# Performance work log

Measured on AMD Instinct MI355X. Metric: run time of the kernel, lower is better.

## Reference

```python
import jax, jax.numpy as jnp
import numpy as np

B, T, D, NH = 2, 2048, 1024, 32
HD = D // NH  # 32
EPS = 1e-6


def rms_norm(x):
    # normalize over head dim in fp32, cast back
    ms = jnp.mean(x.astype(jnp.float32) ** 2, axis=-1, keepdims=True)
    return x * jax.lax.rsqrt(ms + EPS).astype(x.dtype)


def apply_rope(x, cos, sin):
    d = x.shape[-1] // 2
    x1, x2 = x[..., :d], x[..., d:]
    c = cos[: x.shape[-2], :d]
    s = sin[: x.shape[-2], :d]
    return jnp.concatenate([x1 * c - x2 * s, x2 * c + x1 * s], axis=-1)


def setup_inputs() -> dict:
    key = jax.random.key(0)
    ks = jax.random.split(key, 5)
    sc = 1.0 / np.sqrt(D)
    x = jax.random.normal(ks[0], (B, T, D), jnp.float32)
    Wq = jax.random.normal(ks[1], (D, D), jnp.float32) * sc
    Wk = jax.random.normal(ks[2], (NH * HD, D), jnp.float32) * sc
    Wv = jax.random.normal(ks[3], (NH * HD, D), jnp.float32) * sc
    Wproj = jax.random.normal(ks[4], (D, D), jnp.float32) * sc
    q_gain = jnp.ones((NH,), jnp.float32)  # qk_gain = 1.0
    # real RoPE tables, shape [T, HD//2]
    pos = np.arange(T, dtype=np.float32)
    inv = 1.0 / (10000.0 ** (np.arange(HD // 2, dtype=np.float32) / (HD // 2)))
    ang = pos[:, None] * inv[None, :]
    cos = jnp.asarray(np.cos(ang), jnp.float32)
    sin = jnp.asarray(np.sin(ang), jnp.float32)
    return {"x": x, "Wq": Wq, "Wk": Wk, "Wv": Wv, "Wproj": Wproj,
            "q_gain": q_gain, "cos": cos, "sin": sin}


def reference(x, Wq, Wk, Wv, Wproj, q_gain, cos, sin):
    Bx, Tx, Dx = x.shape
    nh = q_gain.shape[0]
    hd = Dx // nh
    # projections -> [B, H, T, hd]
    q = (x @ Wq.T).reshape(Bx, Tx, nh, hd).transpose(0, 2, 1, 3)
    k = (x @ Wk.T).reshape(Bx, Tx, nh, hd).transpose(0, 2, 1, 3)
    v = (x @ Wv.T).reshape(Bx, Tx, nh, hd).transpose(0, 2, 1, 3)
    q = apply_rope(rms_norm(q), cos, sin) * q_gain[None, :, None, None]
    k = apply_rope(rms_norm(k), cos, sin)
    scale = hd ** (-0.5)
    scores = jnp.einsum('bhqd,bhkd->bhqk', q, k) * scale
    causal = jnp.tril(jnp.ones((Tx, Tx), bool))
    scores = jnp.where(causal, scores, jnp.finfo(scores.dtype).min)
    attn = jax.nn.softmax(scores, axis=-1)
    y = jnp.einsum('bhqk,bhkd->bhqd', attn, v)
    y = y.transpose(0, 2, 1, 3).reshape(Bx, Tx, Dx)
    return y @ Wproj.T
```

## Files before the change

kernel.cpp:

```cpp
#include <hip/hip_runtime.h>

#define DEV __device__ __forceinline__

typedef __bf16 bf16x8 __attribute__((ext_vector_type(8)));
typedef float f32x4 __attribute__((ext_vector_type(4)));

static constexpr int Tn = 2048;
static constexpr int Dn = 1024;
static constexpr int NHn = 32;
static constexpr int Mn = 2 * Tn;
static constexpr float QSCALE = 0.17677669529663687f * 1.4426950408889634f;

DEV unsigned short f2bf(float f) {
    unsigned int u = __builtin_bit_cast(unsigned int, f);
    u = u + 0x7FFFu + ((u >> 16) & 1u);
    return (unsigned short)(u >> 16);
}

#define GPTR(p) ((const __attribute__((address_space(1))) void*)(p))
#define LPTR(p) ((__attribute__((address_space(3))) void*)(p))

__global__ __launch_bounds__(256) void cast_all(
    const float* __restrict__ x, const float* __restrict__ Wq, const float* __restrict__ Wk,
    const float* __restrict__ Wv, const float* __restrict__ Wp,
    unsigned short* __restrict__ xb, unsigned short* __restrict__ wall) {
    int i = blockIdx.x * 256 + threadIdx.x;
    const float* src;
    ushort4* dst;
    if (i < (1 << 20)) {
        src = x + (size_t)i * 4;
        dst = reinterpret_cast<ushort4*>(xb) + i;
    } else {
        int j = i - (1 << 20);
        int sel = j >> 18, off = j & ((1 << 18) - 1);
        const float* w = (sel == 0) ? Wq : (sel == 1) ? Wk : (sel == 2) ? Wv : Wp;
        src = w + (size_t)off * 4;
        dst = reinterpret_cast<ushort4*>(wall) + ((size_t)sel << 18) + off;
    }
    float4 v = *reinterpret_cast<const float4*>(src);
    ushort4 o;
    o.x = f2bf(v.x); o.y = f2bf(v.y); o.z = f2bf(v.z); o.w = f2bf(v.w);
    *dst = o;
}

__global__ __launch_bounds__(256) void gemm_qkv(
    const unsigned short* __restrict__ A, const unsigned short* __restrict__ Wall,
    unsigned short* __restrict__ Qn, unsigned short* __restrict__ Kn, unsigned short* __restrict__ Vt,
    const float* __restrict__ gain, const float* __restrict__ cosp, const float* __restrict__ sinp) {
    const int z = blockIdx.z;
    const unsigned short* Bm = Wall + (size_t)z * (Dn * Dn);
    const int m0 = blockIdx.x * 128, n0 = blockIdx.y * 128;
    const int tid = threadIdx.x, w = tid >> 6, l = tid & 63;
    const int wm = w & 1, wn = w >> 1, lm = l & 15, quad = l >> 4;

    __shared__ __align__(16) unsigned short As[128 * 32];
    __shared__ __align__(16) unsigned short Bs[128 * 32];

    f32x4 acc[4][4] = {};

    const int r0 = (w * 2 + 0) * 16 + (l >> 2);
    const int r1 = (w * 2 + 1) * 16 + (l >> 2);
    const int c0 = (l & 3) * 8;
    const unsigned short* gA0 = A + (long)(m0 + r0) * Dn + c0;
    const unsigned short* gA1 = A + (long)(m0 + r1) * Dn + c0;
    const unsigned short* gB0 = Bm + (long)(n0 + r0) * Dn + c0;
    const unsigned short* gB1 = Bm + (long)(n0 + r1) * Dn + c0;
    unsigned short* lA0 = As + (w * 2 + 0) * 16 * 32;
    unsigned short* lA1 = As + (w * 2 + 1) * 16 * 32;
    unsigned short* lB0 = Bs + (w * 2 + 0) * 16 * 32;
    unsigned short* lB1 = Bs + (w * 2 + 1) * 16 * 32;

    for (int kk = 0; kk < Dn; kk += 32) {
        __builtin_amdgcn_global_load_lds(GPTR(gA0 + kk), LPTR(lA0), 16, 0, 0);
        __builtin_amdgcn_global_load_lds(GPTR(gA1 + kk), LPTR(lA1), 16, 0, 0);
        __builtin_amdgcn_global_load_lds(GPTR(gB0 + kk), LPTR(lB0), 16, 0, 0);
        __builtin_amdgcn_global_load_lds(GPTR(gB1 + kk), LPTR(lB1), 16, 0, 0);
        __syncthreads();
        bf16x8 af[4], bfv[4];
#pragma unroll
        for (int mt = 0; mt < 4; ++mt)
            af[mt] = __builtin_bit_cast(bf16x8,
                *reinterpret_cast<const uint4*>(As + (wm * 64 + mt * 16 + lm) * 32 + quad * 8));
#pragma unroll
        for (int nt = 0; nt < 4; ++nt)
            bfv[nt] = __builtin_bit_cast(bf16x8,
                *reinterpret_cast<const uint4*>(Bs + (wn * 64 + nt * 16 + lm) * 32 + quad * 8));
#pragma unroll
        for (int mt = 0; mt < 4; ++mt)
#pragma unroll
            for (int nt = 0; nt < 4; ++nt)
                acc[mt][nt] = __builtin_amdgcn_mfma_f32_16x16x32_bf16(af[mt], bfv[nt], acc[mt][nt], 0, 0, 0);
        __syncthreads();
    }

    if (z == 2) {
#pragma unroll
        for (int mt = 0; mt < 4; ++mt) {
            int row0 = m0 + wm * 64 + mt * 16 + quad * 4;
            int b_ = row0 >> 11, t_ = row0 & (Tn - 1);
#pragma unroll
            for (int nt = 0; nt < 4; ++nt) {
                int col = n0 + wn * 64 + nt * 16 + lm;
                int hh = col >> 5, dd = col & 31;
                ushort4 o4;
                o4.x = f2bf(acc[mt][nt][0]); o4.y = f2bf(acc[mt][nt][1]);
                o4.z = f2bf(acc[mt][nt][2]); o4.w = f2bf(acc[mt][nt][3]);
                *reinterpret_cast<ushort4*>(&Vt[((long)(b_ * NHn + hh) * 32 + dd) * Tn + t_]) = o4;
            }
        }
    } else {
        unsigned short* dst = z ? Kn : Qn;
#pragma unroll
        for (int mt = 0; mt < 4; ++mt)
#pragma unroll
            for (int r = 0; r < 4; ++r) {
                int row = m0 + wm * 64 + mt * 16 + quad * 4 + r;
                int b_ = row >> 11, t_ = row & (Tn - 1);
                float c = cosp[t_ * 16 + lm], s = sinp[t_ * 16 + lm];
#pragma unroll
                for (int g = 0; g < 2; ++g) {
                    float x1 = acc[mt][2 * g][r], x2 = acc[mt][2 * g + 1][r];
                    float ssv = x1 * x1 + x2 * x2;
#pragma unroll
                    for (int off = 8; off >= 1; off >>= 1) ssv += __shfl_xor(ssv, off, 16);
                    float rinv = rsqrtf(ssv * (1.0f / 32.0f) + 1e-6f);
                    x1 *= rinv; x2 *= rinv;
                    float o1 = x1 * c - x2 * s;
                    float o2 = x2 * c + x1 * s;
                    int hh = (n0 + wn * 64 + g * 32) >> 5;
                    if (z == 0) { float gs = gain[hh] * QSCALE; o1 *= gs; o2 *= gs; }
                    long base = ((long)(b_ * NHn + hh) * Tn + t_) * 32;
                    dst[base + lm] = f2bf(o1);
                    dst[base + 16 + lm] = f2bf(o2);
                }
            }
    }
}

__global__ __launch_bounds__(256) void gemm_proj(
    const unsigned short* __restrict__ A, const unsigned short* __restrict__ Bm,
    float* __restrict__ C) {
    const int m0 = blockIdx.x * 128, n0 = blockIdx.y * 128;
    const int tid = threadIdx.x, w = tid >> 6, l = tid & 63;
    const int wm = w & 1, wn = w >> 1, lm = l & 15, quad = l >> 4;

    __shared__ __align__(16) unsigned short As[128 * 32];
    __shared__ __align__(16) unsigned short Bs[128 * 32];

    f32x4 acc[4][4] = {};

    const int r0 = (w * 2 + 0) * 16 + (l >> 2);
    const int r1 = (w * 2 + 1) * 16 + (l >> 2);
    const int c0 = (l & 3) * 8;
    const unsigned short* gA0 = A + (long)(m0 + r0) * Dn + c0;
    const unsigned short* gA1 = A + (long)(m0 + r1) * Dn + c0;
    const unsigned short* gB0 = Bm + (long)(n0 + r0) * Dn + c0;
    const unsigned short* gB1 = Bm + (long)(n0 + r1) * Dn + c0;
    unsigned short* lA0 = As + (w * 2 + 0) * 16 * 32;
    unsigned short* lA1 = As + (w * 2 + 1) * 16 * 32;
    unsigned short* lB0 = Bs + (w * 2 + 0) * 16 * 32;
    unsigned short* lB1 = Bs + (w * 2 + 1) * 16 * 32;

    for (int kk = 0; kk < Dn; kk += 32) {
        __builtin_amdgcn_global_load_lds(GPTR(gA0 + kk), LPTR(lA0), 16, 0, 0);
        __builtin_amdgcn_global_load_lds(GPTR(gA1 + kk), LPTR(lA1), 16, 0, 0);
        __builtin_amdgcn_global_load_lds(GPTR(gB0 + kk), LPTR(lB0), 16, 0, 0);
        __builtin_amdgcn_global_load_lds(GPTR(gB1 + kk), LPTR(lB1), 16, 0, 0);
        __syncthreads();
        bf16x8 af[4], bfv[4];
#pragma unroll
        for (int mt = 0; mt < 4; ++mt)
            af[mt] = __builtin_bit_cast(bf16x8,
                *reinterpret_cast<const uint4*>(As + (wm * 64 + mt * 16 + lm) * 32 + quad * 8));
#pragma unroll
        for (int nt = 0; nt < 4; ++nt)
            bfv[nt] = __builtin_bit_cast(bf16x8,
                *reinterpret_cast<const uint4*>(Bs + (wn * 64 + nt * 16 + lm) * 32 + quad * 8));
#pragma unroll
        for (int mt = 0; mt < 4; ++mt)
#pragma unroll
            for (int nt = 0; nt < 4; ++nt)
                acc[mt][nt] = __builtin_amdgcn_mfma_f32_16x16x32_bf16(af[mt], bfv[nt], acc[mt][nt], 0, 0, 0);
        __syncthreads();
    }
#pragma unroll
    for (int mt = 0; mt < 4; ++mt)
#pragma unroll
        for (int nt = 0; nt < 4; ++nt)
#pragma unroll
            for (int r = 0; r < 4; ++r) {
                int rg = m0 + wm * 64 + mt * 16 + quad * 4 + r;
                int cg = n0 + wn * 64 + nt * 16 + lm;
                C[(long)rg * Dn + cg] = acc[mt][nt][r];
            }
}

__global__ __launch_bounds__(256) void attn(
    const unsigned short* __restrict__ Qn, const unsigned short* __restrict__ Kn,
    const unsigned short* __restrict__ Vt, unsigned short* __restrict__ Y) {
    const int bx = blockIdx.x, h = blockIdx.y, b = blockIdx.z;
    const int tid = threadIdx.x, w = tid >> 6, l = tid & 63;
    const int lm = l & 15, quad = l >> 4;
    const long bh = b * NHn + h;
    const unsigned short* Qh = Qn + bh * Tn * 32;
    const unsigned short* Kh = Kn + bh * Tn * 32;
    const unsigned short* Vh = Vt + bh * 32 * Tn;
    __shared__ __align__(16) unsigned short Pl[4][16][76];
    unsigned short* Pw = &Pl[w][0][0];

    for (int pass = 0; pass < 2; ++pass) {
        const int qb = pass ? (15 - bx) : bx;
        const int q0 = qb * 128 + w * 32;

        bf16x8 qf[2];
        float negM[2][4];
        float lpart[2][4] = {};
        f32x4 o[2][2] = {{{0.f, 0.f, 0.f, 0.f}, {0.f, 0.f, 0.f, 0.f}},
                         {{0.f, 0.f, 0.f, 0.f}, {0.f, 0.f, 0.f, 0.f}}};
#pragma unroll
        for (int t = 0; t < 2; ++t) {
            qf[t] = __builtin_bit_cast(bf16x8,
                *reinterpret_cast<const uint4*>(Qh + (q0 + t * 16 + lm) * 32 + quad * 8));
            float ss = 0.f;
#pragma unroll
            for (int j = 0; j < 8; ++j) { float v = (float)qf[t][j]; ss += v * v; }
            ss += __shfl_xor(ss, 16);
            ss += __shfl_xor(ss, 32);
            float Mv = __builtin_sqrtf(ss * 32.0f);
#pragma unroll
            for (int r = 0; r < 4; ++r) negM[t][r] = -__shfl(Mv, quad * 4 + r, 16);
        }

        const int kend = q0 + 31;
        uint4 ka[4], va[4], kb2[4], vb2[4];

        auto load_t = [&](uint4* kd, uint4* vd, int k0) {
#pragma unroll
            for (int i = 0; i < 4; ++i)
                kd[i] = *reinterpret_cast<const uint4*>(Kh + (k0 + i * 16 + lm) * 32 + quad * 8);
#pragma unroll
            for (int kf2 = 0; kf2 < 2; ++kf2)
#pragma unroll
                for (int nh_ = 0; nh_ < 2; ++nh_)
                    vd[kf2 * 2 + nh_] = *reinterpret_cast<const uint4*>(
                        Vh + (nh_ * 16 + lm) * Tn + k0 + kf2 * 32 + quad * 8);
        };

        auto compute_t = [&](const uint4* kd, const uint4* vd, int k0) {
#pragma unroll
            for (int t = 0; t < 2; ++t) {
                if (k0 > q0 + t * 16 + 15) continue;
                f32x4 s[4];
#pragma unroll
                for (int i = 0; i < 4; ++i) {
                    f32x4 zz = {0.f, 0.f, 0.f, 0.f};
                    s[i] = __builtin_amdgcn_mfma_f32_16x16x32_bf16(
                        qf[t], __builtin_bit_cast(bf16x8, kd[i]), zz, 0, 0, 0);
                }
                const bool full = (k0 + 63) <= (q0 + t * 16);
#pragma unroll
                for (int r = 0; r < 4; ++r) {
                    const int qrow = q0 + t * 16 + quad * 4 + r;
                    const float nm = negM[t][r];
                    float ls = lpart[t][r];
#pragma unroll
                    for (int i = 0; i < 4; ++i) {
                        float p = __builtin_amdgcn_exp2f(s[i][r] + nm);
                        if (!full) {
                            int kc = k0 + i * 16 + lm;
                            p = (kc <= qrow) ? p : 0.0f;
                        }
                        s[i][r] = p;
                        ls += p;
                    }
                    lpart[t][r] = ls;
                }
#pragma unroll
                for (int i = 0; i < 4; ++i)
#pragma unroll
                    for (int r = 0; r < 4; ++r)
                        Pw[(quad * 4 + r) * 76 + i * 16 + lm] = f2bf(s[i][r]);
#pragma unroll
                for (int kf2 = 0; kf2 < 2; ++kf2) {
                    bf16x8 pf = __builtin_bit_cast(bf16x8,
                        *reinterpret_cast<const uint4*>(Pw + lm * 76 + kf2 * 32 + quad * 8));
#pragma unroll
                    for (int nh_ = 0; nh_ < 2; ++nh_)
                        o[t][nh_] = __builtin_amdgcn_mfma_f32_16x16x32_bf16(
                            pf, __builtin_bit_cast(bf16x8, vd[kf2 * 2 + nh_]), o[t][nh_], 0, 0, 0);
                }
            }
        };

        load_t(ka, va, 0);
        int k0 = 0;
        while (true) {
            int nk = k0 + 64;
            if (nk <= kend) load_t(kb2, vb2, nk);
            compute_t(ka, va, k0);
            if (nk > kend) break;
            k0 = nk;
            nk = k0 + 64;
            if (nk <= kend) load_t(ka, va, nk);
            compute_t(kb2, vb2, k0);
            if (nk > kend) break;
            k0 = nk;
        }

#pragma unroll
        for (int t = 0; t < 2; ++t)
#pragma unroll
            for (int r = 0; r < 4; ++r) {
                float ls = lpart[t][r];
#pragma unroll
                for (int off = 8; off >= 1; off >>= 1) ls += __shfl_xor(ls, off, 16);
                float inv = 1.0f / ls;
                int qrow = q0 + t * 16 + quad * 4 + r;
                long base = ((long)(b * Tn + qrow) * NHn + h) * 32;
                Y[base + lm] = f2bf(o[t][0][r] * inv);
                Y[base + 16 + lm] = f2bf(o[t][1][r] * inv);
            }
    }
}

extern "C" void kernel_launch(void* const* d_in, const int* in_sizes, int n_in,
                              void* d_out, int out_size, void* d_ws, size_t ws_size,
                              hipStream_t stream) {
    (void)in_sizes; (void)n_in; (void)out_size; (void)ws_size;
    const float* x = (const float*)d_in[0];
    const float* Wq = (const float*)d_in[1];
    const float* Wk = (const float*)d_in[2];
    const float* Wv = (const float*)d_in[3];
    const float* Wp = (const float*)d_in[4];
    const float* gain = (const float*)d_in[5];
    const float* cosp = (const float*)d_in[6];
    const float* sinp = (const float*)d_in[7];

    char* ws = (char*)d_ws;
    const size_t SZ = (size_t)Mn * Dn * 2;
    unsigned short* xb = (unsigned short*)ws;
    unsigned short* wall = (unsigned short*)(ws + SZ);
    unsigned short* qn = (unsigned short*)(ws + 2 * SZ);
    unsigned short* kn = qn + (size_t)Mn * Dn;
    unsigned short* vt = kn + (size_t)Mn * Dn;
    unsigned short* ybuf = vt + (size_t)Mn * Dn;

    cast_all<<<8192, 256, 0, stream>>>(x, Wq, Wk, Wv, Wp, xb, wall);

    gemm_qkv<<<dim3(Mn / 128, Dn / 128, 3), 256, 0, stream>>>(
        xb, wall, qn, kn, vt, gain, cosp, sinp);

    attn<<<dim3(8, NHn, 2), 256, 0, stream>>>(qn, kn, vt, ybuf);

    gemm_proj<<<dim3(Mn / 128, Dn / 128), 256, 0, stream>>>(
        ybuf, wall + (size_t)3 * Dn * Dn, (float*)d_out);
}
```

Measured before the change: 213.7 us.

## Compute transposed scores in registers, drop LDS P staging, split attention blocks

The attention kernel now computes S^T (K as the A operand), so the probabilities come out already laid out as the A operand for the PV MFMA. This removes the shared-memory round trip for P. It also launches one query block per workgroup (16 per head, heaviest first) instead of pairing two blocks per workgroup, and loads V per tile inside compute rather than double-buffering it. Separately, gemm_proj uses 128x64 tiles for more blocks, and both GEMMs get a min-blocks-per-CU launch bound. The risks are more register pressure in the GEMMs and exposed V load latency in attention.

Measured after the change: 291.5 us. 1.36x slower.

```diff
diff --git a/kernel.cpp b/kernel.cpp
--- a/kernel.cpp
+++ b/kernel.cpp
@@ -4,6 +4,7 @@
 
 typedef __bf16 bf16x8 __attribute__((ext_vector_type(8)));
 typedef float f32x4 __attribute__((ext_vector_type(4)));
+typedef short short8v __attribute__((ext_vector_type(8)));
 
 static constexpr int Tn = 2048;
 static constexpr int Dn = 1024;
@@ -43,7 +44,7 @@
     *dst = o;
 }
 
-__global__ __launch_bounds__(256) void gemm_qkv(
+__global__ __launch_bounds__(256, 3) void gemm_qkv(
     const unsigned short* __restrict__ A, const unsigned short* __restrict__ Wall,
     unsigned short* __restrict__ Qn, unsigned short* __restrict__ Kn, unsigned short* __restrict__ Vt,
     const float* __restrict__ gain, const float* __restrict__ cosp, const float* __restrict__ sinp) {
@@ -137,60 +138,58 @@
     }
 }
 
-__global__ __launch_bounds__(256) void gemm_proj(
+__global__ __launch_bounds__(256, 3) void gemm_proj(
     const unsigned short* __restrict__ A, const unsigned short* __restrict__ Bm,
     float* __restrict__ C) {
-    const int m0 = blockIdx.x * 128, n0 = blockIdx.y * 128;
+    const int m0 = blockIdx.x * 128, n0 = blockIdx.y * 64;
     const int tid = threadIdx.x, w = tid >> 6, l = tid & 63;
     const int wm = w & 1, wn = w >> 1, lm = l & 15, quad = l >> 4;
 
     __shared__ __align__(16) unsigned short As[128 * 32];
-    __shared__ __align__(16) unsigned short Bs[128 * 32];
-
-    f32x4 acc[4][4] = {};
+    __shared__ __align__(16) unsigned short Bs[64 * 32];
+
+    f32x4 acc[4][2] = {};
 
     const int r0 = (w * 2 + 0) * 16 + (l >> 2);
     const int r1 = (w * 2 + 1) * 16 + (l >> 2);
+    const int rb = w * 16 + (l >> 2);
     const int c0 = (l & 3) * 8;
     const unsigned short* gA0 = A + (long)(m0 + r0) * Dn + c0;
     const unsigned short* gA1 = A + (long)(m0 + r1) * Dn + c0;
-    const unsigned short* gB0 = Bm + (long)(n0 + r0) * Dn + c0;
-    const unsigned short* gB1 = Bm + (long)(n0 + r1) * Dn + c0;
+    const unsigned short* gB0 = Bm + (long)(n0 + rb) * Dn + c0;
     unsigned short* lA0 = As + (w * 2 + 0) * 16 * 32;
     unsigned short* lA1 = As + (w * 2 + 1) * 16 * 32;
-    unsigned short* lB0 = Bs + (w * 2 + 0) * 16 * 32;
-    unsigned short* lB1 = Bs + (w * 2 + 1) * 16 * 32;
+    unsigned short* lB0 = Bs + w * 16 * 32;
 
     for (int kk = 0; kk < Dn; kk += 32) {
         __builtin_amdgcn_global_load_lds(GPTR(gA0 + kk), LPTR(lA0), 16, 0, 0);
         __builtin_amdgcn_global_load_lds(GPTR(gA1 + kk), LPTR(lA1), 16, 0, 0);
         __builtin_amdgcn_global_load_lds(GPTR(gB0 + kk), LPTR(lB0), 16, 0, 0);
-        __builtin_amdgcn_global_load_lds(GPTR(gB1 + kk), LPTR(lB1), 16, 0, 0);
         __syncthreads();
-        bf16x8 af[4], bfv[4];
+        bf16x8 af[4], bfv[2];
 #pragma unroll
         for (int mt = 0; mt < 4; ++mt)
             af[mt] = __builtin_bit_cast(bf16x8,
                 *reinterpret_cast<const uint4*>(As + (wm * 64 + mt * 16 + lm) * 32 + quad * 8));
 #pragma unroll
-        for (int nt = 0; nt < 4; ++nt)
+        for (int nt = 0; nt < 2; ++nt)
             bfv[nt] = __builtin_bit_cast(bf16x8,
-                *reinterpret_cast<const uint4*>(Bs + (wn * 64 + nt * 16 + lm) * 32 + quad * 8));
-#pragma unroll
-        for (int mt = 0; mt < 4; ++mt)
-#pragma unroll
-            for (int nt = 0; nt < 4; ++nt)
+                *reinterpret_cast<const uint4*>(Bs + (wn * 32 + nt * 16 + lm) * 32 + quad * 8));
+#pragma unroll
+        for (int mt = 0; mt < 4; ++mt)
+#pragma unroll
+            for (int nt = 0; nt < 2; ++nt)
                 acc[mt][nt] = __builtin_amdgcn_mfma_f32_16x16x32_bf16(af[mt], bfv[nt], acc[mt][nt], 0, 0, 0);
         __syncthreads();
     }
 #pragma unroll
     for (int mt = 0; mt < 4; ++mt)
 #pragma unroll
-        for (int nt = 0; nt < 4; ++nt)
+        for (int nt = 0; nt < 2; ++nt)
 #pragma unroll
             for (int r = 0; r < 4; ++r) {
                 int rg = m0 + wm * 64 + mt * 16 + quad * 4 + r;
-                int cg = n0 + wn * 64 + nt * 16 + lm;
+                int cg = n0 + wn * 32 + nt * 16 + lm;
                 C[(long)rg * Dn + cg] = acc[mt][nt][r];
             }
 }
@@ -198,128 +197,118 @@
 __global__ __launch_bounds__(256) void attn(
     const unsigned short* __restrict__ Qn, const unsigned short* __restrict__ Kn,
     const unsigned short* __restrict__ Vt, unsigned short* __restrict__ Y) {
-    const int bx = blockIdx.x, h = blockIdx.y, b = blockIdx.z;
+    const int qb = 15 - blockIdx.x, h = blockIdx.y, b = blockIdx.z;
     const int tid = threadIdx.x, w = tid >> 6, l = tid & 63;
     const int lm = l & 15, quad = l >> 4;
+    const int q0 = qb * 128 + w * 32;
     const long bh = b * NHn + h;
     const unsigned short* Qh = Qn + bh * Tn * 32;
     const unsigned short* Kh = Kn + bh * Tn * 32;
     const unsigned short* Vh = Vt + bh * 32 * Tn;
-    __shared__ __align__(16) unsigned short Pl[4][16][76];
-    unsigned short* Pw = &Pl[w][0][0];
-
-    for (int pass = 0; pass < 2; ++pass) {
-        const int qb = pass ? (15 - bx) : bx;
-        const int q0 = qb * 128 + w * 32;
-
-        bf16x8 qf[2];
-        float negM[2][4];
-        float lpart[2][4] = {};
-        f32x4 o[2][2] = {{{0.f, 0.f, 0.f, 0.f}, {0.f, 0.f, 0.f, 0.f}},
-                         {{0.f, 0.f, 0.f, 0.f}, {0.f, 0.f, 0.f, 0.f}}};
+
+    bf16x8 qf[2];
+    float negM[2], lpart[2] = {0.f, 0.f};
+    f32x4 o[2][2] = {{{0.f, 0.f, 0.f, 0.f}, {0.f, 0.f, 0.f, 0.f}},
+                     {{0.f, 0.f, 0.f, 0.f}, {0.f, 0.f, 0.f, 0.f}}};
+#pragma unroll
+    for (int t = 0; t < 2; ++t) {
+        qf[t] = __builtin_bit_cast(bf16x8,
+            *reinterpret_cast<const uint4*>(Qh + (q0 + t * 16 + lm) * 32 + quad * 8));
+        float ss = 0.f;
+#pragma unroll
+        for (int j = 0; j < 8; ++j) { float v = (float)qf[t][j]; ss += v * v; }
+        ss += __shfl_xor(ss, 16);
+        ss += __shfl_xor(ss, 32);
+        negM[t] = -__builtin_sqrtf(ss * 32.0f);
+    }
+
+    const int kend = q0 + 31;
+    uint4 ka[4], kb[4];
+
+    auto load_k = [&](uint4* kd, int k0) {
+#pragma unroll
+        for (int i = 0; i < 4; ++i)
+            kd[i] = *reinterpret_cast<const uint4*>(Kh + (k0 + i * 16 + lm) * 32 + quad * 8);
+    };
+
+    auto compute_t = [&](const uint4* kd, int k0) {
+        uint2 vd[8];
+#pragma unroll
+        for (int i = 0; i < 4; ++i)
+#pragma unroll
+            for (int nh_ = 0; nh_ < 2; ++nh_)
+                vd[i * 2 + nh_] = *reinterpret_cast<const uint2*>(
+                    Vh + (nh_ * 16 + lm) * Tn + k0 + i * 16 + quad * 4);
 #pragma unroll
         for (int t = 0; t < 2; ++t) {
-            qf[t] = __builtin_bit_cast(bf16x8,
-                *reinterpret_cast<const uint4*>(Qh + (q0 + t * 16 + lm) * 32 + quad * 8));
-            float ss = 0.f;
-#pragma unroll
-            for (int j = 0; j < 8; ++j) { float v = (float)qf[t][j]; ss += v * v; }
-            ss += __shfl_xor(ss, 16);
-            ss += __shfl_xor(ss, 32);
-            float Mv = __builtin_sqrtf(ss * 32.0f);
-#pragma unroll
-            for (int r = 0; r < 4; ++r) negM[t][r] = -__shfl(Mv, quad * 4 + r, 16);
+            if (k0 > q0 + t * 16 + 15) continue;
+            const int qrow = q0 + t * 16 + lm;
+            f32x4 s[4];
+#pragma unroll
+            for (int i = 0; i < 4; ++i) {
+                f32x4 zz = {0.f, 0.f, 0.f, 0.f};
+                s[i] = __builtin_amdgcn_mfma_f32_16x16x32_bf16(
+                    __builtin_bit_cast(bf16x8, kd[i]), qf[t], zz, 0, 0, 0);
+            }
+            const bool full = (k0 + 63) <= (q0 + t * 16);
+            const float nm = negM[t];
+            float ls = lpart[t];
+            short8v pk[2];
+#pragma unroll
+            for (int i = 0; i < 4; ++i)
+#pragma unroll
+                for (int r = 0; r < 4; ++r) {
+                    float p = __builtin_amdgcn_exp2f(s[i][r] + nm);
+                    if (!full) {
+                        int kc = k0 + i * 16 + quad * 4 + r;
+                        p = (kc <= qrow) ? p : 0.0f;
+                    }
+                    ls += p;
+                    pk[i >> 1][(i & 1) * 4 + r] = (short)f2bf(p);
+                }
+            lpart[t] = ls;
+#pragma unroll
+            for (int kh = 0; kh < 2; ++kh) {
+                bf16x8 pa = __builtin_bit_cast(bf16x8, pk[kh]);
+#pragma unroll
+                for (int nh_ = 0; nh_ < 2; ++nh_) {
+                    uint2 b0 = vd[(2 * kh) * 2 + nh_], b1 = vd[(2 * kh + 1) * 2 + nh_];
+                    uint4 bb = {b0.x, b0.y, b1.x, b1.y};
+                    o[t][nh_] = __builtin_amdgcn_mfma_f32_16x16x32_bf16(
+                        pa, __builtin_bit_cast(bf16x8, bb), o[t][nh_], 0, 0, 0);
+                }
+            }
         }
-
-        const int kend = q0 + 31;
-        uint4 ka[4], va[4], kb2[4], vb2[4];
-
-        auto load_t = [&](uint4* kd, uint4* vd, int k0) {
-#pragma unroll
-            for (int i = 0; i < 4; ++i)
-                kd[i] = *reinterpret_cast<const uint4*>(Kh + (k0 + i * 16 + lm) * 32 + quad * 8);
-#pragma unroll
-            for (int kf2 = 0; kf2 < 2; ++kf2)
-#pragma unroll
-                for (int nh_ = 0; nh_ < 2; ++nh_)
-                    vd[kf2 * 2 + nh_] = *reinterpret_cast<const uint4*>(
-                        Vh + (nh_ * 16 + lm) * Tn + k0 + kf2 * 32 + quad * 8);
-        };
-
-        auto compute_t = [&](const uint4* kd, const uint4* vd, int k0) {
-#pragma unroll
-            for (int t = 0; t < 2; ++t) {
-                if (k0 > q0 + t * 16 + 15) continue;
-                f32x4 s[4];
-#pragma unroll
-                for (int i = 0; i < 4; ++i) {
-                    f32x4 zz = {0.f, 0.f, 0.f, 0.f};
-                    s[i] = __builtin_amdgcn_mfma_f32_16x16x32_bf16(
-                        qf[t], __builtin_bit_cast(bf16x8, kd[i]), zz, 0, 0, 0);
-                }
-                const bool full = (k0 + 63) <= (q0 + t * 16);
-#pragma unroll
-                for (int r = 0; r < 4; ++r) {
-                    const int qrow = q0 + t * 16 + quad * 4 + r;
-                    const float nm = negM[t][r];
-                    float ls = lpart[t][r];
-#pragma unroll
-                    for (int i = 0; i < 4; ++i) {
-                        float p = __builtin_amdgcn_exp2f(s[i][r] + nm);
-                        if (!full) {
-                            int kc = k0 + i * 16 + lm;
-                            p = (kc <= qrow) ? p : 0.0f;
-                        }
-                        s[i][r] = p;
-                        ls += p;
-                    }
-                    lpart[t][r] = ls;
-                }
-#pragma unroll
-                for (int i = 0; i < 4; ++i)
-#pragma unroll
-                    for (int r = 0; r < 4; ++r)
-                        Pw[(quad * 4 + r) * 76 + i * 16 + lm] = f2bf(s[i][r]);
-#pragma unroll
-                for (int kf2 = 0; kf2 < 2; ++kf2) {
-                    bf16x8 pf = __builtin_bit_cast(bf16x8,
-                        *reinterpret_cast<const uint4*>(Pw + lm * 76 + kf2 * 32 + quad * 8));
-#pragma unroll
-                    for (int nh_ = 0; nh_ < 2; ++nh_)
-                        o[t][nh_] = __builtin_amdgcn_mfma_f32_16x16x32_bf16(
-                            pf, __builtin_bit_cast(bf16x8, vd[kf2 * 2 + nh_]), o[t][nh_], 0, 0, 0);
-                }
-            }
-        };
-
-        load_t(ka, va, 0);
-        int k0 = 0;
-        while (true) {
-            int nk = k0 + 64;
-            if (nk <= kend) load_t(kb2, vb2, nk);
-            compute_t(ka, va, k0);
-            if (nk > kend) break;
-            k0 = nk;
-            nk = k0 + 64;
-            if (nk <= kend) load_t(ka, va, nk);
-            compute_t(kb2, vb2, k0);
-            if (nk > kend) break;
-            k0 = nk;
+    };
+
+    load_k(ka, 0);
+    int k0 = 0;
+    while (true) {
+        int nk = k0 + 64;
+        if (nk <= kend) load_k(kb, nk);
+        compute_t(ka, k0);
+        if (nk > kend) break;
+        k0 = nk;
+        nk = k0 + 64;
+        if (nk <= kend) load_k(ka, nk);
+        compute_t(kb, k0);
+        if (nk > kend) break;
+        k0 = nk;
+    }
+
+#pragma unroll
+    for (int t = 0; t < 2; ++t) {
+        float lsum = lpart[t];
+        lsum += __shfl_xor(lsum, 16);
+        lsum += __shfl_xor(lsum, 32);
+#pragma unroll
+        for (int r = 0; r < 4; ++r) {
+            float inv = 1.0f / __shfl(lsum, quad * 4 + r, 16);
+            int qrow = q0 + t * 16 + quad * 4 + r;
+            long base = ((long)(b * Tn + qrow) * NHn + h) * 32;
+            Y[base + lm] = f2bf(o[t][0][r] * inv);
+            Y[base + 16 + lm] = f2bf(o[t][1][r] * inv);
         }
-
-#pragma unroll
-        for (int t = 0; t < 2; ++t)
-#pragma unroll
-            for (int r = 0; r < 4; ++r) {
-                float ls = lpart[t][r];
-#pragma unroll
-                for (int off = 8; off >= 1; off >>= 1) ls += __shfl_xor(ls, off, 16);
-                float inv = 1.0f / ls;
-                int qrow = q0 + t * 16 + quad * 4 + r;
-                long base = ((long)(b * Tn + qrow) * NHn + h) * 32;
-                Y[base + lm] = f2bf(o[t][0][r] * inv);
-                Y[base + 16 + lm] = f2bf(o[t][1][r] * inv);
-            }
     }
 }
 
@@ -350,8 +339,8 @@
     gemm_qkv<<<dim3(Mn / 128, Dn / 128, 3), 256, 0, stream>>>(
         xb, wall, qn, kn, vt, gain, cosp, sinp);
 
-    attn<<<dim3(8, NHn, 2), 256, 0, stream>>>(qn, kn, vt, ybuf);
-
-    gemm_proj<<<dim3(Mn / 128, Dn / 128), 256, 0, stream>>>(
+    attn<<<dim3(16, NHn, 2), 256, 0, stream>>>(qn, kn, vt, ybuf);
+
+    gemm_proj<<<dim3(Mn / 128, Dn / 64), 256, 0, stream>>>(
         ybuf, wall + (size_t)3 * Dn * Dn, (float*)d_out);
 }
```

## Split attention KV range across warp pairs, shrink proj tiles, add occupancy bounds

Applied to the files above, without the earlier changes.

The attention kernel now gives each block 64 query rows. Two warp pairs split the causal key blocks between them in an interleaved way, and their partial outputs and row sums are merged through shared memory. The grid doubles to improve load balance and CU fill. The P-tile bf16 conversion uses a cheaper round-half-up. The output projection GEMM uses 128x64 tiles to launch more blocks, and launch-bound occupancy hints are added to the GEMMs and attention. The trade-offs are extra sync and reduction work, more register pressure from the occupancy hints, and a slightly different rounding.

New measurement: 271.1 us. +26.8%, slower.

```diff
diff --git a/kernel.cpp b/kernel.cpp
--- a/kernel.cpp
+++ b/kernel.cpp
@@ -15,6 +15,10 @@
     unsigned int u = __builtin_bit_cast(unsigned int, f);
     u = u + 0x7FFFu + ((u >> 16) & 1u);
     return (unsigned short)(u >> 16);
+}
+DEV unsigned short f2bf_fast(float f) {
+    unsigned int u = __builtin_bit_cast(unsigned int, f);
+    return (unsigned short)((u + 0x8000u) >> 16);
 }
 
 #define GPTR(p) ((const __attribute__((address_space(1))) void*)(p))
@@ -43,7 +47,7 @@
     *dst = o;
 }
 
-__global__ __launch_bounds__(256) void gemm_qkv(
+__global__ __launch_bounds__(256, 3) void gemm_qkv(
     const unsigned short* __restrict__ A, const unsigned short* __restrict__ Wall,
     unsigned short* __restrict__ Qn, unsigned short* __restrict__ Kn, unsigned short* __restrict__ Vt,
     const float* __restrict__ gain, const float* __restrict__ cosp, const float* __restrict__ sinp) {
@@ -137,80 +141,80 @@
     }
 }
 
-__global__ __launch_bounds__(256) void gemm_proj(
+__global__ __launch_bounds__(256, 3) void gemm_proj(
     const unsigned short* __restrict__ A, const unsigned short* __restrict__ Bm,
     float* __restrict__ C) {
-    const int m0 = blockIdx.x * 128, n0 = blockIdx.y * 128;
+    const int m0 = blockIdx.x * 128, n0 = blockIdx.y * 64;
     const int tid = threadIdx.x, w = tid >> 6, l = tid & 63;
     const int wm = w & 1, wn = w >> 1, lm = l & 15, quad = l >> 4;
 
     __shared__ __align__(16) unsigned short As[128 * 32];
-    __shared__ __align__(16) unsigned short Bs[128 * 32];
-
-    f32x4 acc[4][4] = {};
+    __shared__ __align__(16) unsigned short Bs[64 * 32];
+
+    f32x4 acc[4][2] = {};
 
     const int r0 = (w * 2 + 0) * 16 + (l >> 2);
     const int r1 = (w * 2 + 1) * 16 + (l >> 2);
+    const int rb = w * 16 + (l >> 2);
     const int c0 = (l & 3) * 8;
     const unsigned short* gA0 = A + (long)(m0 + r0) * Dn + c0;
     const unsigned short* gA1 = A + (long)(m0 + r1) * Dn + c0;
-    const unsigned short* gB0 = Bm + (long)(n0 + r0) * Dn + c0;
-    const unsigned short* gB1 = Bm + (long)(n0 + r1) * Dn + c0;
+    const unsigned short* gB0 = Bm + (long)(n0 + rb) * Dn + c0;
     unsigned short* lA0 = As + (w * 2 + 0) * 16 * 32;
     unsigned short* lA1 = As + (w * 2 + 1) * 16 * 32;
-    unsigned short* lB0 = Bs + (w * 2 + 0) * 16 * 32;
-    unsigned short* lB1 = Bs + (w * 2 + 1) * 16 * 32;
+    unsigned short* lB0 = Bs + w * 16 * 32;
 
     for (int kk = 0; kk < Dn; kk += 32) {
         __builtin_amdgcn_global_load_lds(GPTR(gA0 + kk), LPTR(lA0), 16, 0, 0);
         __builtin_amdgcn_global_load_lds(GPTR(gA1 + kk), LPTR(lA1), 16, 0, 0);
         __builtin_amdgcn_global_load_lds(GPTR(gB0 + kk), LPTR(lB0), 16, 0, 0);
-        __builtin_amdgcn_global_load_lds(GPTR(gB1 + kk), LPTR(lB1), 16, 0, 0);
-        __syncthreads();
-        bf16x8 af[4], bfv[4];
+        __syncthreads();
+        bf16x8 af[4], bfv[2];
 #pragma unroll
         for (int mt = 0; mt < 4; ++mt)
             af[mt] = __builtin_bit_cast(bf16x8,
                 *reinterpret_cast<const uint4*>(As + (wm * 64 + mt * 16 + lm) * 32 + quad * 8));
 #pragma unroll
-        for (int nt = 0; nt < 4; ++nt)
+        for (int nt = 0; nt < 2; ++nt)
             bfv[nt] = __builtin_bit_cast(bf16x8,
-                *reinterpret_cast<const uint4*>(Bs + (wn * 64 + nt * 16 + lm) * 32 + quad * 8));
-#pragma unroll
-        for (int mt = 0; mt < 4; ++mt)
-#pragma unroll
-            for (int nt = 0; nt < 4; ++nt)
+                *reinterpret_cast<const uint4*>(Bs + (wn * 32 + nt * 16 + lm) * 32 + quad * 8));
+#pragma unroll
+        for (int mt = 0; mt < 4; ++mt)
+#pragma unroll
+            for (int nt = 0; nt < 2; ++nt)
                 acc[mt][nt] = __builtin_amdgcn_mfma_f32_16x16x32_bf16(af[mt], bfv[nt], acc[mt][nt], 0, 0, 0);
         __syncthreads();
     }
 #pragma unroll
     for (int mt = 0; mt < 4; ++mt)
 #pragma unroll
-        for (int nt = 0; nt < 4; ++nt)
+        for (int nt = 0; nt < 2; ++nt)
 #pragma unroll
             for (int r = 0; r < 4; ++r) {
                 int rg = m0 + wm * 64 + mt * 16 + quad * 4 + r;
-                int cg = n0 + wn * 64 + nt * 16 + lm;
+                int cg = n0 + wn * 32 + nt * 16 + lm;
                 C[(long)rg * Dn + cg] = acc[mt][nt][r];
             }
 }
 
-__global__ __launch_bounds__(256) void attn(
+__global__ __launch_bounds__(256, 4) void attn(
     const unsigned short* __restrict__ Qn, const unsigned short* __restrict__ Kn,
     const unsigned short* __restrict__ Vt, unsigned short* __restrict__ Y) {
     const int bx = blockIdx.x, h = blockIdx.y, b = blockIdx.z;
     const int tid = threadIdx.x, w = tid >> 6, l = tid & 63;
+    const int rg = w & 1, sp = w >> 1;
     const int lm = l & 15, quad = l >> 4;
     const long bh = b * NHn + h;
     const unsigned short* Qh = Qn + bh * Tn * 32;
     const unsigned short* Kh = Kn + bh * Tn * 32;
     const unsigned short* Vh = Vt + bh * 32 * Tn;
     __shared__ __align__(16) unsigned short Pl[4][16][76];
+    __shared__ float cbuf[2][64][24];
     unsigned short* Pw = &Pl[w][0][0];
 
     for (int pass = 0; pass < 2; ++pass) {
-        const int qb = pass ? (15 - bx) : bx;
-        const int q0 = qb * 128 + w * 32;
+        const int qb = pass ? bx : 31 - bx;
+        const int q0 = qb * 64 + rg * 32;
 
         bf16x8 qf[2];
         float negM[2][4];
@@ -231,8 +235,7 @@
             for (int r = 0; r < 4; ++r) negM[t][r] = -__shfl(Mv, quad * 4 + r, 16);
         }
 
-        const int kend = q0 + 31;
-        uint4 ka[4], va[4], kb2[4], vb2[4];
+        uint4 ka[4], kb[4], va[4], vb[4];
 
         auto load_t = [&](uint4* kd, uint4* vd, int k0) {
 #pragma unroll
@@ -257,29 +260,28 @@
                     s[i] = __builtin_amdgcn_mfma_f32_16x16x32_bf16(
                         qf[t], __builtin_bit_cast(bf16x8, kd[i]), zz, 0, 0, 0);
                 }
-                const bool full = (k0 + 63) <= (q0 + t * 16);
-#pragma unroll
-                for (int r = 0; r < 4; ++r) {
-                    const int qrow = q0 + t * 16 + quad * 4 + r;
-                    const float nm = negM[t][r];
-                    float ls = lpart[t][r];
-#pragma unroll
-                    for (int i = 0; i < 4; ++i) {
-                        float p = __builtin_amdgcn_exp2f(s[i][r] + nm);
-                        if (!full) {
+                if ((k0 + 63) <= (q0 + t * 16)) {
+#pragma unroll
+                    for (int i = 0; i < 4; ++i)
+#pragma unroll
+                        for (int r = 0; r < 4; ++r) {
+                            float p = __builtin_amdgcn_exp2f(s[i][r] + negM[t][r]);
+                            lpart[t][r] += p;
+                            Pw[(quad * 4 + r) * 76 + i * 16 + lm] = f2bf_fast(p);
+                        }
+                } else {
+#pragma unroll
+                    for (int i = 0; i < 4; ++i)
+#pragma unroll
+                        for (int r = 0; r < 4; ++r) {
+                            int qrow = q0 + t * 16 + quad * 4 + r;
                             int kc = k0 + i * 16 + lm;
+                            float p = __builtin_amdgcn_exp2f(s[i][r] + negM[t][r]);
                             p = (kc <= qrow) ? p : 0.0f;
+                            lpart[t][r] += p;
+                            Pw[(quad * 4 + r) * 76 + i * 16 + lm] = f2bf_fast(p);
                         }
-                        s[i][r] = p;
-                        ls += p;
-                    }
-                    lpart[t][r] = ls;
-                }
-#pragma unroll
-                for (int i = 0; i < 4; ++i)
-#pragma unroll
-                    for (int r = 0; r < 4; ++r)
-                        Pw[(quad * 4 + r) * 76 + i * 16 + lm] = f2bf(s[i][r]);
+                }
 #pragma unroll
                 for (int kf2 = 0; kf2 < 2; ++kf2) {
                     bf16x8 pf = __builtin_bit_cast(bf16x8,
@@ -292,34 +294,59 @@
             }
         };
 
-        load_t(ka, va, 0);
-        int k0 = 0;
-        while (true) {
-            int nk = k0 + 64;
-            if (nk <= kend) load_t(kb2, vb2, nk);
-            compute_t(ka, va, k0);
-            if (nk > kend) break;
-            k0 = nk;
-            nk = k0 + 64;
-            if (nk <= kend) load_t(ka, va, nk);
-            compute_t(kb2, vb2, k0);
-            if (nk > kend) break;
-            k0 = nk;
-        }
-
-#pragma unroll
-        for (int t = 0; t < 2; ++t)
-#pragma unroll
-            for (int r = 0; r < 4; ++r) {
-                float ls = lpart[t][r];
-#pragma unroll
-                for (int off = 8; off >= 1; off >>= 1) ls += __shfl_xor(ls, off, 16);
-                float inv = 1.0f / ls;
-                int qrow = q0 + t * 16 + quad * 4 + r;
-                long base = ((long)(b * Tn + qrow) * NHn + h) * 32;
-                Y[base + lm] = f2bf(o[t][0][r] * inv);
-                Y[base + 16 + lm] = f2bf(o[t][1][r] * inv);
-            }
+        int j = sp;
+        if (j <= qb) {
+            load_t(ka, va, j * 64);
+            while (true) {
+                int jn = j + 2;
+                if (jn <= qb) load_t(kb, vb, jn * 64);
+                compute_t(ka, va, j * 64);
+                if (jn > qb) break;
+                j = jn;
+                jn = j + 2;
+                if (jn <= qb) load_t(ka, va, jn * 64);
+                compute_t(kb, vb, j * 64);
+                if (jn > qb) break;
+                j = jn;
+            }
+        }
+
+        if (sp == 1) {
+            float* cb = &cbuf[rg][l][0];
+#pragma unroll
+            for (int t = 0; t < 2; ++t)
+#pragma unroll
+                for (int nh_ = 0; nh_ < 2; ++nh_)
+#pragma unroll
+                    for (int r = 0; r < 4; ++r) cb[t * 8 + nh_ * 4 + r] = o[t][nh_][r];
+#pragma unroll
+            for (int t = 0; t < 2; ++t)
+#pragma unroll
+                for (int r = 0; r < 4; ++r) cb[16 + t * 4 + r] = lpart[t][r];
+        }
+        __syncthreads();
+        if (sp == 0) {
+            const float* cb = &cbuf[rg][l][0];
+#pragma unroll
+            for (int t = 0; t < 2; ++t) {
+#pragma unroll
+                for (int nh_ = 0; nh_ < 2; ++nh_)
+#pragma unroll
+                    for (int r = 0; r < 4; ++r) o[t][nh_][r] += cb[t * 8 + nh_ * 4 + r];
+#pragma unroll
+                for (int r = 0; r < 4; ++r) {
+                    float ls = lpart[t][r] + cb[16 + t * 4 + r];
+#pragma unroll
+                    for (int off = 8; off >= 1; off >>= 1) ls += __shfl_xor(ls, off, 16);
+                    float inv = 1.0f / ls;
+                    int qr = q0 + t * 16 + quad * 4 + r;
+                    long base = ((long)(b * Tn + qr) * NHn + h) * 32;
+                    Y[base + lm] = f2bf(o[t][0][r] * inv);
+                    Y[base + 16 + lm] = f2bf(o[t][1][r] * inv);
+                }
+            }
+        }
+        __syncthreads();
     }
 }
 
@@ -350,8 +377,8 @@
     gemm_qkv<<<dim3(Mn / 128, Dn / 128, 3), 256, 0, stream>>>(
         xb, wall, qn, kn, vt, gain, cosp, sinp);
 
-    attn<<<dim3(8, NHn, 2), 256, 0, stream>>>(qn, kn, vt, ybuf);
-
-    gemm_proj<<<dim3(Mn / 128, Dn / 128), 256, 0, stream>>>(
+    attn<<<dim3(16, NHn, 2), 256, 0, stream>>>(qn, kn, vt, ybuf);
+
+    gemm_proj<<<dim3(Mn / 128, Dn / 64), 256, 0, stream>>>(
         ybuf, wall + (size_t)3 * Dn * Dn, (float*)d_out);
 }
```
